# Kernel tuning notes

Measured on AMD Instinct MI355X. Metric: run time of the kernel, lower is better.

## Reference

```python
import jax, jax.numpy as jnp
import numpy as np

B, L, D = 8, 4096, 1024


def setup_inputs() -> dict:
    key = jax.random.key(0)
    k1, k2, k3 = jax.random.split(key, 3)
    scale = 1.0 / np.sqrt(D)  # ~xavier magnitude for DxD
    return {
        "x": jax.random.normal(k1, (B, L, D), dtype=jnp.float32),
        "hidden": jnp.zeros((B, D), dtype=jnp.float32),
        "Wg": jax.random.normal(k2, (D, D), dtype=jnp.float32) * scale,
        "bg": jnp.ones((D,), dtype=jnp.float32),  # gate bias init = 1.0
        "Wh": jax.random.normal(k3, (D, D), dtype=jnp.float32) * scale,
        "bh": jnp.zeros((D,), dtype=jnp.float32),
    }


def reference(x, hidden, Wg, bg, Wh, bh):
    # g_t = sigmoid(x W_g^T + b_g); c_t = tanh(x W_h^T + b_h)
    g = jax.nn.sigmoid(jnp.einsum('bld,ed->ble', x, Wg) + bg)
    c = jnp.tanh(jnp.einsum('bld,ed->ble', x, Wh) + bh)
    # linear recurrence h_t = a_t * h_{t-1} + b_t with a=g, b=(1-g)*c
    a = g
    b = (1.0 - g) * c

    def combine(left, right):
        al, bl = left
        ar, br = right
        return ar * al, ar * bl + br

    A, Bv = jax.lax.associative_scan(combine, (a, b), axis=1)
    # h_t = A_t * h0 + B_t  (cumulative affine map applied to init hidden)
    return A * hidden[:, None, :] + Bv
```

## Files before the change

kernel.cpp:

```cpp
#include <hip/hip_runtime.h>
#include <hip/hip_bf16.h>
#include <cstdint>


using u16   = unsigned short;
using f32x4 = __attribute__((ext_vector_type(4))) float;
using h16x4 = __attribute__((ext_vector_type(4))) _Float16;
using h16x8 = __attribute__((ext_vector_type(8))) _Float16;

#define M_TOTAL 32768
#define K_DIM   1024
#define E_DIM   1024
#define LCH     32
#define NCH     128

__global__ void conv_w(const float* __restrict__ wg, const float* __restrict__ wh,
                       u16* __restrict__ dst_base, int n4) {
    const float* w = blockIdx.y ? wh : wg;
    u16* dst = dst_base + (size_t)blockIdx.y * 1024 * 1024;
    int i = blockIdx.x * blockDim.x + threadIdx.x;
    if (i >= n4) return;
    f32x4 f = ((const f32x4*)w)[i];
    h16x4 h;
#pragma unroll
    for (int c = 0; c < 4; ++c) h[c] = (_Float16)f[c];
    ((h16x4*)dst)[i] = h;
}

__device__ inline float fast_sigmoid(float z) {
    return 1.f / (1.f + __expf(-z));
}
__device__ inline float fast_tanh(float z) {
    return 1.f - 2.f / (__expf(2.f * z) + 1.f);
}

__global__ __launch_bounds__(256, 2) void gemm_act(
    const float* __restrict__ x,
    const u16* __restrict__ wg_h, const u16* __restrict__ wh_h,
    const float* __restrict__ bg, const float* __restrict__ bh,
    _Float16* __restrict__ g_out, _Float16* __restrict__ c_out) {

    const int e0 = blockIdx.x * 128;
    const int m0 = blockIdx.y * 128;

    __shared__ __align__(16) union SM {
        struct {
            u16 A[128 * 40];
            u16 B[2][128 * 32];
        } s;
        float tile[128][132];
    } sm;

    const int tid  = threadIdx.x;
    const int lane = tid & 63;
    const int wave = tid >> 6;
    const int wr = wave >> 1, wc = wave & 1;
    const int lr = lane & 15;
    const int kg = lane >> 4;

    const u16* __restrict__ Wptr[2] = {wg_h, wh_h};

    f32x4 accg[4][4], acch[4][4];
#pragma unroll
    for (int tr = 0; tr < 4; ++tr)
#pragma unroll
        for (int tc = 0; tc < 4; ++tc) {
            accg[tr][tc] = (f32x4){0.f, 0.f, 0.f, 0.f};
            acch[tr][tc] = (f32x4){0.f, 0.f, 0.f, 0.f};
        }

    for (int kt = 0; kt < K_DIM / 32; ++kt) {
        __syncthreads();

#pragma unroll
        for (int rgn = 0; rgn < 2; ++rgn) {
#pragma unroll
            for (int j = 0; j < 2; ++j) {
                int ch  = tid + 256 * j;
                int row = ch >> 2;
                int kq  = ch & 3;
                int kqs = kq ^ ((row >> 1) & 3);
                size_t goff = (size_t)(e0 + row) * K_DIM + kt * 32 + kqs * 8;
                __builtin_amdgcn_global_load_lds(
                    (const __attribute__((address_space(1))) void*)(Wptr[rgn] + goff),
                    (__attribute__((address_space(3))) void*)(&sm.s.B[rgn][ch * 8]), 16, 0, 0);
            }
        }

#pragma unroll
        for (int j = 0; j < 4; ++j) {
            int q   = tid + 256 * j;
            int row = q >> 3;
            int kq  = q & 7;
            f32x4 f = *(const f32x4*)(x + (size_t)(m0 + row) * K_DIM + kt * 32 + kq * 4);
            h16x4 h;
#pragma unroll
            for (int c = 0; c < 4; ++c) h[c] = (_Float16)f[c];
            *(h16x4*)&sm.s.A[row * 40 + kq * 4] = h;
        }

        __syncthreads();

        h16x8 ah[4];
#pragma unroll
        for (int tr = 0; tr < 4; ++tr) {
            int r = wr * 64 + tr * 16 + lr;
            ah[tr] = *(const h16x8*)&sm.s.A[r * 40 + kg * 8];
        }
#pragma unroll
        for (int tc = 0; tc < 4; ++tc) {
            int e   = wc * 64 + tc * 16 + lr;
            int kgs = kg ^ ((e >> 1) & 3);
            h16x8 bgv = *(const h16x8*)&sm.s.B[0][e * 32 + kgs * 8];
            h16x8 bhv = *(const h16x8*)&sm.s.B[1][e * 32 + kgs * 8];
#pragma unroll
            for (int tr = 0; tr < 4; ++tr) {
                accg[tr][tc] = __builtin_amdgcn_mfma_f32_16x16x32_f16(ah[tr], bgv, accg[tr][tc], 0, 0, 0);
                acch[tr][tc] = __builtin_amdgcn_mfma_f32_16x16x32_f16(ah[tr], bhv, acch[tr][tc], 0, 0, 0);
            }
        }
    }

#pragma unroll
    for (int arr = 0; arr < 2; ++arr) {
        __syncthreads();
#pragma unroll
        for (int tc = 0; tc < 4; ++tc) {
            int el = wc * 64 + tc * 16 + lr;
            float bv = (arr ? bh : bg)[e0 + el];
#pragma unroll
            for (int tr = 0; tr < 4; ++tr) {
                int rb = wr * 64 + tr * 16 + kg * 4;
#pragma unroll
                for (int i = 0; i < 4; ++i) {
                    float z = (arr ? acch : accg)[tr][tc][i] + bv;
                    sm.tile[rb + i][el] = arr ? fast_tanh(z) : fast_sigmoid(z);
                }
            }
        }
        __syncthreads();
        _Float16* outp = arr ? c_out : g_out;
#pragma unroll
        for (int p = 0; p < 8; ++p) {
            int row = p * 16 + (tid >> 4);
            int c8  = (tid & 15) * 8;
            f32x4 v0 = *(const f32x4*)&sm.tile[row][c8];
            f32x4 v1 = *(const f32x4*)&sm.tile[row][c8 + 4];
            h16x8 hv;
#pragma unroll
            for (int j = 0; j < 4; ++j) { hv[j] = (_Float16)v0[j]; hv[j + 4] = (_Float16)v1[j]; }
            *(h16x8*)(outp + (size_t)(m0 + row) * E_DIM + e0 + c8) = hv;
        }
    }
}

__global__ void chunk_compose(const _Float16* __restrict__ g_arr,
                              const _Float16* __restrict__ c_arr,
                              float* __restrict__ Ac, float* __restrict__ Bc) {
    int d4 = threadIdx.x * 4;
    int ch = blockIdx.x;
    int b  = blockIdx.y;
    size_t base = ((size_t)b * 4096 + (size_t)ch * LCH) * 1024 + d4;
    float A[4] = {1.f, 1.f, 1.f, 1.f}, Bv[4] = {0.f, 0.f, 0.f, 0.f};
#pragma unroll 8
    for (int t = 0; t < LCH; ++t) {
        h16x4 gv = *(const h16x4*)(g_arr + base + (size_t)t * 1024);
        h16x4 cv = *(const h16x4*)(c_arr + base + (size_t)t * 1024);
#pragma unroll
        for (int j = 0; j < 4; ++j) {
            float g = (float)gv[j];
            float c = (float)cv[j];
            A[j]  = g * A[j];
            Bv[j] = g * Bv[j] + (1.f - g) * c;
        }
    }
    size_t o = ((size_t)b * NCH + ch) * 1024 + d4;
    *(f32x4*)(Ac + o) = (f32x4){A[0], A[1], A[2], A[3]};
    *(f32x4*)(Bc + o) = (f32x4){Bv[0], Bv[1], Bv[2], Bv[3]};
}

__global__ void chunk_prefix(const float* __restrict__ Ac, const float* __restrict__ Bc,
                             const float* __restrict__ hidden, float* __restrict__ Hst) {
    int idx = blockIdx.x * 256 + threadIdx.x;
    int b = idx >> 10;
    int d = idx & 1023;
    float h = hidden[b * 1024 + d];
#pragma unroll 8
    for (int ch = 0; ch < NCH; ++ch) {
        size_t o = ((size_t)b * NCH + ch) * 1024 + d;
        float A = Ac[o], Bv = Bc[o];
        Hst[o] = h;
        h = A * h + Bv;
    }
}

__global__ void chunk_apply(const _Float16* __restrict__ g_arr,
                            const _Float16* __restrict__ c_arr,
                            const float* __restrict__ Hst,
                            float* __restrict__ out) {
    int d4 = threadIdx.x * 4;
    int ch = blockIdx.x;
    int b  = blockIdx.y;
    size_t base = ((size_t)b * 4096 + (size_t)ch * LCH) * 1024 + d4;
    size_t ho = ((size_t)b * NCH + ch) * 1024 + d4;
    f32x4 hv = *(const f32x4*)(Hst + ho);
    float h[4] = {hv[0], hv[1], hv[2], hv[3]};
#pragma unroll 4
    for (int t = 0; t < LCH; ++t) {
        size_t idx = base + (size_t)t * 1024;
        h16x4 gv = *(const h16x4*)(g_arr + idx);
        h16x4 cv = *(const h16x4*)(c_arr + idx);
#pragma unroll
        for (int j = 0; j < 4; ++j) {
            float g = (float)gv[j];
            float c = (float)cv[j];
            h[j] = g * h[j] + (1.f - g) * c;
        }
        *(f32x4*)(out + idx) = (f32x4){h[0], h[1], h[2], h[3]};
    }
}

extern "C" void kernel_launch(void* const* d_in, const int* in_sizes, int n_in,
                              void* d_out, int out_size, void* d_ws, size_t ws_size,
                              hipStream_t stream) {
    const float* x      = (const float*)d_in[0];
    const float* hidden = (const float*)d_in[1];
    const float* Wg     = (const float*)d_in[2];
    const float* bg     = (const float*)d_in[3];
    const float* Wh     = (const float*)d_in[4];
    const float* bh     = (const float*)d_in[5];
    float* out = (float*)d_out;

    char* ws = (char*)d_ws;
    const size_t WSEG = 2u * 1024u * 1024u;
    u16* wg_h = (u16*)(ws + 0 * WSEG);
    u16* wh_h = (u16*)(ws + 1 * WSEG);
    const size_t HBYTES = (size_t)M_TOTAL * E_DIM * 2;
    _Float16* g_arr = (_Float16*)(ws + 4 * WSEG);
    _Float16* c_arr = (_Float16*)(ws + 4 * WSEG + HBYTES);
    const size_t SSEG = (size_t)8 * NCH * 1024 * 4;
    float* Ac  = (float*)(ws + 4 * WSEG + 2 * HBYTES);
    float* Bc  = (float*)(ws + 4 * WSEG + 2 * HBYTES + SSEG);
    float* Hst = (float*)(ws + 4 * WSEG + 2 * HBYTES + 2 * SSEG);

    conv_w<<<dim3(1024, 2), 256, 0, stream>>>(Wg, Wh, wg_h, (1024 * 1024) / 4);

    gemm_act<<<dim3(E_DIM / 128, M_TOTAL / 128), 256, 0, stream>>>(
        x, wg_h, wh_h, bg, bh, g_arr, c_arr);

    chunk_compose<<<dim3(NCH, 8), 256, 0, stream>>>(g_arr, c_arr, Ac, Bc);
    chunk_prefix<<<dim3(32), 256, 0, stream>>>(Ac, Bc, hidden, Hst);
    chunk_apply<<<dim3(NCH, 8), 256, 0, stream>>>(g_arr, c_arr, Hst, out);
}
```

Measured before the change: 496.7 us.

## Fuse chunk composition into GEMM epilogue with 512-thread blocks and XCD-aware tiling

Moves the per-chunk affine composition into the GEMM epilogue, so the separate kernel that re-read the fp16 g and c arrays from global memory is no longer needed. Blocks grow to 512 threads (8 waves at 64x32 each), and block IDs are remapped so each XCD handles a contiguous range of M tiles for better L2 reuse. The epilogue now stages 32-row slices of g and c together in LDS. The composition runs on only 128 threads per slice, which adds serial work to the tail of the GEMM and may raise register pressure under the new launch bounds.

```diff
diff --git a/kernel.cpp b/kernel.cpp
--- a/kernel.cpp
+++ b/kernel.cpp
@@ -34,37 +34,46 @@
     return 1.f - 2.f / (__expf(2.f * z) + 1.f);
 }
 
-__global__ __launch_bounds__(256, 2) void gemm_act(
+__global__ __launch_bounds__(512, 4) void gemm_act(
     const float* __restrict__ x,
     const u16* __restrict__ wg_h, const u16* __restrict__ wh_h,
     const float* __restrict__ bg, const float* __restrict__ bh,
-    _Float16* __restrict__ g_out, _Float16* __restrict__ c_out) {
-
-    const int e0 = blockIdx.x * 128;
-    const int m0 = blockIdx.y * 128;
+    _Float16* __restrict__ g_out, _Float16* __restrict__ c_out,
+    float* __restrict__ Ac, float* __restrict__ Bc) {
+
+    const int bid   = blockIdx.x;
+    const int xcd   = bid & 7;
+    const int local = bid >> 3;
+    const int mt    = xcd * 32 + (local >> 3);
+    const int et    = local & 7;
+    const int e0    = et * 128;
+    const int m0    = mt * 128;
 
     __shared__ __align__(16) union SM {
         struct {
             u16 A[128 * 40];
             u16 B[2][128 * 32];
         } s;
-        float tile[128][132];
+        struct {
+            float g[32][132];
+            float c[32][132];
+        } ep;
     } sm;
 
     const int tid  = threadIdx.x;
     const int lane = tid & 63;
     const int wave = tid >> 6;
-    const int wr = wave >> 1, wc = wave & 1;
+    const int wr = wave >> 2, wc = wave & 3;
     const int lr = lane & 15;
     const int kg = lane >> 4;
 
     const u16* __restrict__ Wptr[2] = {wg_h, wh_h};
 
-    f32x4 accg[4][4], acch[4][4];
+    f32x4 accg[4][2], acch[4][2];
 #pragma unroll
     for (int tr = 0; tr < 4; ++tr)
 #pragma unroll
-        for (int tc = 0; tc < 4; ++tc) {
+        for (int tc = 0; tc < 2; ++tc) {
             accg[tr][tc] = (f32x4){0.f, 0.f, 0.f, 0.f};
             acch[tr][tc] = (f32x4){0.f, 0.f, 0.f, 0.f};
         }
@@ -74,22 +83,19 @@
 
 #pragma unroll
         for (int rgn = 0; rgn < 2; ++rgn) {
-#pragma unroll
-            for (int j = 0; j < 2; ++j) {
-                int ch  = tid + 256 * j;
-                int row = ch >> 2;
-                int kq  = ch & 3;
-                int kqs = kq ^ ((row >> 1) & 3);
-                size_t goff = (size_t)(e0 + row) * K_DIM + kt * 32 + kqs * 8;
-                __builtin_amdgcn_global_load_lds(
-                    (const __attribute__((address_space(1))) void*)(Wptr[rgn] + goff),
-                    (__attribute__((address_space(3))) void*)(&sm.s.B[rgn][ch * 8]), 16, 0, 0);
-            }
-        }
-
-#pragma unroll
-        for (int j = 0; j < 4; ++j) {
-            int q   = tid + 256 * j;
+            int ch  = tid;
+            int row = ch >> 2;
+            int kq  = ch & 3;
+            int kqs = kq ^ ((row >> 1) & 3);
+            size_t goff = (size_t)(e0 + row) * K_DIM + kt * 32 + kqs * 8;
+            __builtin_amdgcn_global_load_lds(
+                (const __attribute__((address_space(1))) void*)(Wptr[rgn] + goff),
+                (__attribute__((address_space(3))) void*)(&sm.s.B[rgn][ch * 8]), 16, 0, 0);
+        }
+
+#pragma unroll
+        for (int j = 0; j < 2; ++j) {
+            int q   = tid + 512 * j;
             int row = q >> 3;
             int kq  = q & 7;
             f32x4 f = *(const f32x4*)(x + (size_t)(m0 + row) * K_DIM + kt * 32 + kq * 4);
@@ -108,8 +114,8 @@
             ah[tr] = *(const h16x8*)&sm.s.A[r * 40 + kg * 8];
         }
 #pragma unroll
-        for (int tc = 0; tc < 4; ++tc) {
-            int e   = wc * 64 + tc * 16 + lr;
+        for (int tc = 0; tc < 2; ++tc) {
+            int e   = wc * 32 + tc * 16 + lr;
             int kgs = kg ^ ((e >> 1) & 3);
             h16x8 bgv = *(const h16x8*)&sm.s.B[0][e * 32 + kgs * 8];
             h16x8 bhv = *(const h16x8*)&sm.s.B[1][e * 32 + kgs * 8];
@@ -121,62 +127,69 @@
         }
     }
 
-#pragma unroll
-    for (int arr = 0; arr < 2; ++arr) {
-        __syncthreads();
-#pragma unroll
-        for (int tc = 0; tc < 4; ++tc) {
-            int el = wc * 64 + tc * 16 + lr;
-            float bv = (arr ? bh : bg)[e0 + el];
-#pragma unroll
-            for (int tr = 0; tr < 4; ++tr) {
-                int rb = wr * 64 + tr * 16 + kg * 4;
-#pragma unroll
-                for (int i = 0; i < 4; ++i) {
-                    float z = (arr ? acch : accg)[tr][tc][i] + bv;
-                    sm.tile[rb + i][el] = arr ? fast_tanh(z) : fast_sigmoid(z);
+    float bgv[2], bhv[2];
+#pragma unroll
+    for (int tc = 0; tc < 2; ++tc) {
+        int el = e0 + wc * 32 + tc * 16 + lr;
+        bgv[tc] = bg[el];
+        bhv[tc] = bh[el];
+    }
+
+#pragma unroll
+    for (int s = 0; s < 4; ++s) {
+        __syncthreads();
+        if (wr == (s >> 1)) {
+#pragma unroll
+            for (int half = 0; half < 2; ++half) {
+                int tr = (s & 1) * 2 + half;
+#pragma unroll
+                for (int tc = 0; tc < 2; ++tc) {
+                    int el = wc * 32 + tc * 16 + lr;
+#pragma unroll
+                    for (int i = 0; i < 4; ++i) {
+                        int row = half * 16 + kg * 4 + i;
+                        sm.ep.g[row][el] = fast_sigmoid(accg[tr][tc][i] + bgv[tc]);
+                        sm.ep.c[row][el] = fast_tanh(acch[tr][tc][i] + bhv[tc]);
+                    }
                 }
             }
         }
         __syncthreads();
-        _Float16* outp = arr ? c_out : g_out;
-#pragma unroll
-        for (int p = 0; p < 8; ++p) {
-            int row = p * 16 + (tid >> 4);
+
+        {
+            int row = tid >> 4;
             int c8  = (tid & 15) * 8;
-            f32x4 v0 = *(const f32x4*)&sm.tile[row][c8];
-            f32x4 v1 = *(const f32x4*)&sm.tile[row][c8 + 4];
+            size_t gofs = (size_t)(m0 + s * 32 + row) * E_DIM + e0 + c8;
+            f32x4 v0 = *(const f32x4*)&sm.ep.g[row][c8];
+            f32x4 v1 = *(const f32x4*)&sm.ep.g[row][c8 + 4];
             h16x8 hv;
 #pragma unroll
             for (int j = 0; j < 4; ++j) { hv[j] = (_Float16)v0[j]; hv[j + 4] = (_Float16)v1[j]; }
-            *(h16x8*)(outp + (size_t)(m0 + row) * E_DIM + e0 + c8) = hv;
-        }
-    }
-}
-
-__global__ void chunk_compose(const _Float16* __restrict__ g_arr,
-                              const _Float16* __restrict__ c_arr,
-                              float* __restrict__ Ac, float* __restrict__ Bc) {
-    int d4 = threadIdx.x * 4;
-    int ch = blockIdx.x;
-    int b  = blockIdx.y;
-    size_t base = ((size_t)b * 4096 + (size_t)ch * LCH) * 1024 + d4;
-    float A[4] = {1.f, 1.f, 1.f, 1.f}, Bv[4] = {0.f, 0.f, 0.f, 0.f};
+            *(h16x8*)(g_out + gofs) = hv;
+            v0 = *(const f32x4*)&sm.ep.c[row][c8];
+            v1 = *(const f32x4*)&sm.ep.c[row][c8 + 4];
+#pragma unroll
+            for (int j = 0; j < 4; ++j) { hv[j] = (_Float16)v0[j]; hv[j + 4] = (_Float16)v1[j]; }
+            *(h16x8*)(c_out + gofs) = hv;
+        }
+
+        if (tid < 128) {
+            float A = 1.f, Bv = 0.f;
 #pragma unroll 8
-    for (int t = 0; t < LCH; ++t) {
-        h16x4 gv = *(const h16x4*)(g_arr + base + (size_t)t * 1024);
-        h16x4 cv = *(const h16x4*)(c_arr + base + (size_t)t * 1024);
-#pragma unroll
-        for (int j = 0; j < 4; ++j) {
-            float g = (float)gv[j];
-            float c = (float)cv[j];
-            A[j]  = g * A[j];
-            Bv[j] = g * Bv[j] + (1.f - g) * c;
-        }
-    }
-    size_t o = ((size_t)b * NCH + ch) * 1024 + d4;
-    *(f32x4*)(Ac + o) = (f32x4){A[0], A[1], A[2], A[3]};
-    *(f32x4*)(Bc + o) = (f32x4){Bv[0], Bv[1], Bv[2], Bv[3]};
+            for (int t = 0; t < LCH; ++t) {
+                float g = (float)(_Float16)sm.ep.g[t][tid];
+                float c = (float)(_Float16)sm.ep.c[t][tid];
+                A  = g * A;
+                Bv = g * Bv + (1.f - g) * c;
+            }
+            int m_abs = m0 + s * 32;
+            int b  = m_abs >> 12;
+            int ch = (m_abs & 4095) >> 5;
+            size_t o = ((size_t)b * NCH + ch) * 1024 + e0 + tid;
+            Ac[o] = A;
+            Bc[o] = Bv;
+        }
+    }
 }
 
 __global__ void chunk_prefix(const float* __restrict__ Ac, const float* __restrict__ Bc,
@@ -245,10 +258,9 @@
 
     conv_w<<<dim3(1024, 2), 256, 0, stream>>>(Wg, Wh, wg_h, (1024 * 1024) / 4);
 
-    gemm_act<<<dim3(E_DIM / 128, M_TOTAL / 128), 256, 0, stream>>>(
-        x, wg_h, wh_h, bg, bh, g_arr, c_arr);
-
-    chunk_compose<<<dim3(NCH, 8), 256, 0, stream>>>(g_arr, c_arr, Ac, Bc);
+    gemm_act<<<dim3(2048), 512, 0, stream>>>(
+        x, wg_h, wh_h, bg, bh, g_arr, c_arr, Ac, Bc);
+
     chunk_prefix<<<dim3(32), 256, 0, stream>>>(Ac, Bc, hidden, Hst);
     chunk_apply<<<dim3(NCH, 8), 256, 0, stream>>>(g_arr, c_arr, Hst, out);
 }
```

Measured after the change: 529.0 us. 6.5% more time.
